# Kernel optimization log

Measured on AMD Instinct MI355X. Metric: run time of the kernel, lower is better.

## Reference

```python
import jax, jax.numpy as jnp
import numpy as np

N_NODES = 50000
IN_CH = 256
OUT_CH = 128
HID = 2 * OUT_CH  # 256
N_EDGES = 800000


def setup_inputs() -> dict:
    key = jax.random.key(0)
    ks = jax.random.split(key, 12)
    glorot = lambda k, shape: jax.random.normal(k, shape, jnp.float32) * (2.0 / sum(shape)) ** 0.5
    return {
        "x": jax.random.normal(ks[0], (N_NODES, IN_CH), jnp.float32),
        "edge_index": jax.random.randint(ks[1], (2, N_EDGES), 0, N_NODES),
        "conv_w": glorot(ks[2], (IN_CH, HID)),      # MetaGCNConv weight: x @ W
        "conv_b": jnp.zeros((HID,), jnp.float32),
        "fc1_w": glorot(ks[3], (HID, HID)), "fc1_b": jnp.zeros((HID,), jnp.float32),
        "fc2_w": glorot(ks[4], (HID, HID)), "fc2_b": jnp.zeros((HID,), jnp.float32),
        "fc3_w": glorot(ks[5], (OUT_CH, HID)), "fc3_b": jnp.zeros((OUT_CH,), jnp.float32),
        "fc4_w": glorot(ks[6], (OUT_CH, HID)), "fc4_b": jnp.zeros((OUT_CH,), jnp.float32),
    }


def reference(x, edge_index, conv_w, conv_b, fc1_w, fc1_b, fc2_w, fc2_b, fc3_w, fc3_b, fc4_w, fc4_b):
    N = x.shape[0]
    # GCN with added self-loops and symmetric normalization (PyG GCNConv semantics)
    loop = jnp.arange(N)
    src = jnp.concatenate([edge_index[0], loop])
    dst = jnp.concatenate([edge_index[1], loop])
    xw = x @ conv_w  # [N, HID]
    ones = jnp.ones_like(src, dtype=x.dtype)
    deg = jax.ops.segment_sum(ones, src, num_segments=N)
    dinv = jnp.where(deg > 0, jax.lax.rsqrt(deg), 0.0)
    norm = dinv[src] * dinv[dst]  # [E+N]
    agg = jax.ops.segment_sum(norm[:, None] * xw[src], dst, num_segments=N)  # [N, HID]
    h = jax.nn.relu(agg + conv_b)
    s = h.sum(0)  # [HID]
    lin = lambda v, w, b: jnp.tanh(v @ w.T + b)
    return (lin(s, fc1_w, fc1_b), lin(s, fc2_w, fc2_b), lin(s, fc3_w, fc3_b), lin(s, fc4_w, fc4_b))
```

## Files before the change

kernel.cpp:

```cpp
#include <hip/hip_runtime.h>
#include <math.h>

#define CH 256
#define BCAP 64

typedef short bf16x8 __attribute__((ext_vector_type(8)));
typedef float f32x4 __attribute__((ext_vector_type(4)));
typedef unsigned int u32;

__device__ __forceinline__ unsigned short f2bf(float f) {
    u32 u = __float_as_uint(f);
    u += 0x7FFFu + ((u >> 16) & 1u);
    return (unsigned short)(u >> 16);
}
__device__ __forceinline__ float bf2f(unsigned short h) {
    return __uint_as_float(((u32)h) << 16);
}
__device__ __forceinline__ float lo16f(u32 q) { return __uint_as_float(q << 16); }
__device__ __forceinline__ float hi16f(u32 q) { return __uint_as_float(q & 0xffff0000u); }
__device__ __forceinline__ u32 pkbf(float a, float b) {
    u32 ua = __float_as_uint(a) + 0x8000u;
    u32 ub = __float_as_uint(b) + 0x8000u;
    return __builtin_amdgcn_perm(ub, ua, 0x07060302u);
}
__device__ __forceinline__ void async16(const void* g, void* l) {
    __builtin_amdgcn_global_load_lds((const __attribute__((address_space(1))) u32*)g,
                                     (__attribute__((address_space(3))) u32*)l, 16, 0, 0);
}

__global__ __launch_bounds__(256) void prep_kernel(const float* __restrict__ W,
                                                   unsigned short* __restrict__ whiT,
                                                   unsigned short* __restrict__ wloT,
                                                   float4* __restrict__ zbase,
                                                   int zcount4) {
    int b = blockIdx.x, t = threadIdx.x;
    if (b < 64) {
#pragma unroll
        for (int i = 0; i < 4; i++) {
            int n = b * 4 + i;
            float w = W[(size_t)t * CH + n];
            unsigned short hi = f2bf(w);
            unsigned short lo = f2bf(w - bf2f(hi));
            whiT[(size_t)n * CH + t] = hi;
            wloT[(size_t)n * CH + t] = lo;
        }
    } else {
        int i = (b - 64) * 256 + t;
        int stride = 104 * 256;
        float4 z = make_float4(0.f, 0.f, 0.f, 0.f);
        for (; i < zcount4; i += stride) zbase[i] = z;
    }
}

__global__ __launch_bounds__(256) void mega_kernel(const float* __restrict__ x,
                                                   const unsigned short* __restrict__ whiT,
                                                   const unsigned short* __restrict__ wloT,
                                                   const int* __restrict__ ei,
                                                   unsigned* __restrict__ cnt_src,
                                                   unsigned* __restrict__ cnt_dst,
                                                   unsigned* __restrict__ col,
                                                   unsigned short* __restrict__ y,
                                                   int M, int E, int G) {
    int b = blockIdx.x, t = threadIdx.x;
    if (b < 2 * G && !(b & 1)) {
        __shared__ __align__(16) unsigned short smA [128 * 32];
        __shared__ __align__(16) unsigned short smBh[128 * 32];
        __shared__ __align__(16) unsigned short smBl[128 * 32];
        int g = b >> 1;
        int lane = t & 63, w = t >> 6;
        int m0 = (g >> 1) * 128;
        int n0 = (g & 1) * 128;
        int mo = (w >> 1) * 64, no = (w & 1) * 64;
        int quad = lane >> 4, l16 = lane & 15;

        f32x4 acc[4][4] = {};

        int arow = t >> 1, ahalf = t & 1;
        int gm = min(m0 + arow, M - 1);
        const float* xrow = x + (size_t)gm * CH + ahalf * 16;
        int idx0 = t, idx1 = t + 256;
        size_t gb0 = (size_t)(n0 + (idx0 >> 2)) * CH + (idx0 & 3) * 8;
        size_t gb1 = (size_t)(n0 + (idx1 >> 2)) * CH + (idx1 & 3) * 8;

        for (int k0 = 0; k0 < CH; k0 += 32) {
            const float4* xp = (const float4*)(xrow + k0);
            float4 v0 = xp[0], v1 = xp[1], v2 = xp[2], v3 = xp[3];
            async16(&whiT[gb0 + k0], &smBh[idx0 * 8]);
            async16(&whiT[gb1 + k0], &smBh[idx1 * 8]);
            async16(&wloT[gb0 + k0], &smBl[idx0 * 8]);
            async16(&wloT[gb1 + k0], &smBl[idx1 * 8]);
            uint4 w0 = make_uint4(pkbf(v0.x, v0.y), pkbf(v0.z, v0.w),
                                  pkbf(v1.x, v1.y), pkbf(v1.z, v1.w));
            uint4 w1 = make_uint4(pkbf(v2.x, v2.y), pkbf(v2.z, v2.w),
                                  pkbf(v3.x, v3.y), pkbf(v3.z, v3.w));
            *(uint4*)&smA[arow * 32 + ahalf * 16]     = w0;
            *(uint4*)&smA[arow * 32 + ahalf * 16 + 8] = w1;
            __syncthreads();

            bf16x8 a[4], bh[4], bl[4];
#pragma unroll
            for (int i = 0; i < 4; i++)
                a[i] = *(const bf16x8*)&smA[(mo + i * 16 + l16) * 32 + quad * 8];
#pragma unroll
            for (int j = 0; j < 4; j++) {
                bh[j] = *(const bf16x8*)&smBh[(no + j * 16 + l16) * 32 + quad * 8];
                bl[j] = *(const bf16x8*)&smBl[(no + j * 16 + l16) * 32 + quad * 8];
            }
#pragma unroll
            for (int i = 0; i < 4; i++)
#pragma unroll
                for (int j = 0; j < 4; j++) {
                    acc[i][j] = __builtin_amdgcn_mfma_f32_16x16x32_bf16(a[i], bh[j], acc[i][j], 0, 0, 0);
                    acc[i][j] = __builtin_amdgcn_mfma_f32_16x16x32_bf16(a[i], bl[j], acc[i][j], 0, 0, 0);
                }
            __syncthreads();
        }
#pragma unroll
        for (int i = 0; i < 4; i++) {
            int mbase = m0 + mo + i * 16 + quad * 4;
#pragma unroll
            for (int r = 0; r < 4; r++) {
                int m = mbase + r;
                if (m < M) {
#pragma unroll
                    for (int j = 0; j < 4; j++) {
                        int ncol = n0 + no + j * 16 + l16;
                        int s = ncol >> 5, c = ncol & 31;
                        y[((size_t)s * M + m) * 32 + c] = f2bf(acc[i][j][r]);
                    }
                }
            }
        }
    } else {
        int fb = (b < 2 * G) ? (b >> 1) : (b - G);
        if (fb >= 1024) return;
        int i = fb * 256 + t;
        int stride = 1024 * 256;
        for (; i < E; i += stride) {
            int s = ei[i];
            int d = ei[E + i];
            atomicAdd(&cnt_src[s], 1u);
            unsigned pos = atomicAdd(&cnt_dst[d], 1u);
            if (pos < BCAP) col[(size_t)d * BCAP + pos] = (unsigned)s;
        }
    }
}

__global__ __launch_bounds__(256) void dinv_kernel(const unsigned* __restrict__ cnt_src,
                                                   float* __restrict__ dinv, int N) {
    int base = (blockIdx.x * 256 + threadIdx.x) * 4;
#pragma unroll
    for (int j = 0; j < 4; j++) {
        int i = base + j;
        if (i < N) dinv[i] = rsqrtf((float)(cnt_src[i] + 1u));
    }
}

__global__ __launch_bounds__(256) void gather_kernel(const unsigned short* __restrict__ y,
                                                     const float* __restrict__ dinv,
                                                     const unsigned* __restrict__ cnt_dst,
                                                     const unsigned* __restrict__ col,
                                                     const float* __restrict__ bias,
                                                     float* __restrict__ s_sum, int N) {
    int t = threadIdx.x;
    int lane = t & 63, wv = t >> 6;
    int slice = blockIdx.x & 7;
    int grp   = blockIdx.x >> 3;
    int ng = lane >> 4;
    int g  = (lane >> 2) & 3;
    int li = lane & 3;
    const unsigned short* ys = y + (size_t)slice * N * 32;

    float b8[8];
#pragma unroll
    for (int j = 0; j < 8; j++) b8[j] = bias[slice * 32 + li * 8 + j];

    float ts[8] = {0.f, 0.f, 0.f, 0.f, 0.f, 0.f, 0.f, 0.f};

    int wid = grp * 4 + wv;
    int nw  = (gridDim.x >> 3) * 4;

    for (int base = wid * 4; base < N; base += nw * 4) {
        int n = min(base + ng, N - 1);
        unsigned deg = min(cnt_dst[n], (unsigned)BCAP);
        unsigned cnt = deg + 1;
        float gnm = (g == 0 && base + ng < N) ? 1.f : 0.f;
        unsigned mc = cnt;
        mc = max(mc, (unsigned)__shfl_xor((int)mc, 16, 64));
        mc = max(mc, (unsigned)__shfl_xor((int)mc, 32, 64));

        const unsigned* cb = col + (size_t)n * BCAP;
        float acc[8] = {0.f, 0.f, 0.f, 0.f, 0.f, 0.f, 0.f, 0.f};
        for (unsigned k = 0; k < mc; k += 4) {
            unsigned r = k + g;
            unsigned src = (r < deg) ? cb[r] : (unsigned)n;
            float wgt = (r < cnt) ? dinv[src] : 0.f;
            uint4 q = *(const uint4*)(ys + (size_t)src * 32 + li * 8);
            acc[0] = fmaf(wgt, lo16f(q.x), acc[0]);
            acc[1] = fmaf(wgt, hi16f(q.x), acc[1]);
            acc[2] = fmaf(wgt, lo16f(q.y), acc[2]);
            acc[3] = fmaf(wgt, hi16f(q.y), acc[3]);
            acc[4] = fmaf(wgt, lo16f(q.z), acc[4]);
            acc[5] = fmaf(wgt, hi16f(q.z), acc[5]);
            acc[6] = fmaf(wgt, lo16f(q.w), acc[6]);
            acc[7] = fmaf(wgt, hi16f(q.w), acc[7]);
        }
        float dvn = dinv[n];
#pragma unroll
        for (int j = 0; j < 8; j++) {
            float v = acc[j];
            v += __shfl_xor(v, 4, 64);
            v += __shfl_xor(v, 8, 64);
            float h = fmaxf(fmaf(dvn, v, b8[j]), 0.f);
            ts[j] = fmaf(gnm, h, ts[j]);
        }
    }

#pragma unroll
    for (int j = 0; j < 8; j++) {
        float v = ts[j];
        v += __shfl_xor(v, 16, 64);
        v += __shfl_xor(v, 32, 64);
        ts[j] = v;
    }

    __shared__ float red[4][32];
    if (lane < 4) {
#pragma unroll
        for (int j = 0; j < 8; j++) red[wv][lane * 8 + j] = ts[j];
    }
    __syncthreads();
    if (t < 32) {
        atomicAdd(&s_sum[slice * 32 + t],
                  red[0][t] + red[1][t] + red[2][t] + red[3][t]);
    }
}

__global__ __launch_bounds__(256) void fc_kernel(const float* __restrict__ s_sum,
                                                 const float* __restrict__ fc1_w, const float* __restrict__ fc1_b,
                                                 const float* __restrict__ fc2_w, const float* __restrict__ fc2_b,
                                                 const float* __restrict__ fc3_w, const float* __restrict__ fc3_b,
                                                 const float* __restrict__ fc4_w, const float* __restrict__ fc4_b,
                                                 float* __restrict__ out) {
    int wid  = (blockIdx.x * blockDim.x + threadIdx.x) >> 6;
    int lane = threadIdx.x & 63;
    if (wid >= 768) return;
    const float* w; const float* b; int row, obase;
    if (wid < 256)      { w = fc1_w; b = fc1_b; row = wid;       obase = 0;   }
    else if (wid < 512) { w = fc2_w; b = fc2_b; row = wid - 256; obase = 256; }
    else if (wid < 640) { w = fc3_w; b = fc3_b; row = wid - 512; obase = 512; }
    else                { w = fc4_w; b = fc4_b; row = wid - 640; obase = 640; }
    float4 wv = *(const float4*)&w[(size_t)row * 256 + lane * 4];
    float4 sv = *(const float4*)&s_sum[lane * 4];
    float d = wv.x * sv.x + wv.y * sv.y + wv.z * sv.z + wv.w * sv.w;
#pragma unroll
    for (int off = 32; off; off >>= 1) d += __shfl_down(d, off, 64);
    if (lane == 0) out[obase + row] = tanhf(d + b[row]);
}

extern "C" void kernel_launch(void* const* d_in, const int* in_sizes, int n_in,
                              void* d_out, int out_size, void* d_ws, size_t ws_size,
                              hipStream_t stream) {
    const float* x      = (const float*)d_in[0];
    const int*   ei     = (const int*)d_in[1];
    const float* conv_w = (const float*)d_in[2];
    const float* conv_b = (const float*)d_in[3];
    const float* fc1_w  = (const float*)d_in[4];
    const float* fc1_b  = (const float*)d_in[5];
    const float* fc2_w  = (const float*)d_in[6];
    const float* fc2_b  = (const float*)d_in[7];
    const float* fc3_w  = (const float*)d_in[8];
    const float* fc3_b  = (const float*)d_in[9];
    const float* fc4_w  = (const float*)d_in[10];
    const float* fc4_b  = (const float*)d_in[11];
    float* out = (float*)d_out;

    const int N = in_sizes[0] / CH;
    const int E = in_sizes[1] / 2;
    const int G = ((N + 127) / 128) * 2;

    char* ws = (char*)d_ws;
    size_t off = 0;
    auto alloc = [&](size_t bytes) -> void* {
        off = (off + 255) & ~(size_t)255;
        void* p = ws + off;
        off += bytes;
        return p;
    };
    unsigned* cnt_src = (unsigned*)alloc((size_t)N * 4);
    unsigned* cnt_dst = (unsigned*)alloc((size_t)N * 4);
    float*    s_sum   = (float*)alloc((size_t)CH * 4);
    size_t zero_bytes = off;
    unsigned* col     = (unsigned*)alloc((size_t)N * BCAP * 4);
    float*    dinv    = (float*)alloc((size_t)N * 4);
    unsigned short* whiT = (unsigned short*)alloc((size_t)CH * CH * 2);
    unsigned short* wloT = (unsigned short*)alloc((size_t)CH * CH * 2);
    unsigned short* y    = (unsigned short*)alloc((size_t)N * CH * 2);

    int zcount4 = (int)((zero_bytes + 15) / 16);

    prep_kernel<<<168, 256, 0, stream>>>(conv_w, whiT, wloT, (float4*)ws, zcount4);
    mega_kernel<<<G + 1024, 256, 0, stream>>>(x, whiT, wloT, ei,
                                              cnt_src, cnt_dst, col, y, N, E, G);
    dinv_kernel<<<(N + 1023) / 1024, 256, 0, stream>>>(cnt_src, dinv, N);
    gather_kernel<<<2048, 256, 0, stream>>>(y, dinv, cnt_dst, col, conv_b, s_sum, N);
    fc_kernel<<<192, 256, 0, stream>>>(s_sum,
                                       fc1_w, fc1_b, fc2_w, fc2_b,
                                       fc3_w, fc3_b, fc4_w, fc4_b, out);
}
```

Baseline: 260.6 us.

## Fuse dinv into gather and run FC layers in last-arriving gather blocks

Removes the separate dinv kernel by computing rsqrt(deg+1) from cnt_src inline during the gather. Also removes the separate FC kernel: each gather block increments a done counter, and the last 8 blocks to arrive spin until all blocks finish, then compute the 768 FC outputs. This saves two kernel launches and the dinv round trip through memory. In exchange the gather does extra rsqrt work and cnt_src lookups, and the tail blocks spin-wait, which is safe only because the waiting blocks are the last to arrive.

```diff
diff --git a/kernel.cpp b/kernel.cpp
--- a/kernel.cpp
+++ b/kernel.cpp
@@ -3,6 +3,7 @@
 
 #define CH 256
 #define BCAP 64
+#define GGRID 2048
 
 typedef short bf16x8 __attribute__((ext_vector_type(8)));
 typedef float f32x4 __attribute__((ext_vector_type(4)));
@@ -28,11 +29,11 @@
                                      (__attribute__((address_space(3))) u32*)l, 16, 0, 0);
 }
 
-__global__ __launch_bounds__(256) void prep_kernel(const float* __restrict__ W,
-                                                   unsigned short* __restrict__ whiT,
-                                                   unsigned short* __restrict__ wloT,
-                                                   float4* __restrict__ zbase,
-                                                   int zcount4) {
+__global__ __launch_bounds__(256) void prep0_kernel(const float* __restrict__ W,
+                                                    unsigned short* __restrict__ whiT,
+                                                    unsigned short* __restrict__ wloT,
+                                                    float4* __restrict__ zbase,
+                                                    int zcount4) {
     int b = blockIdx.x, t = threadIdx.x;
     if (b < 64) {
 #pragma unroll
@@ -46,7 +47,7 @@
         }
     } else {
         int i = (b - 64) * 256 + t;
-        int stride = 104 * 256;
+        int stride = 64 * 256;
         float4 z = make_float4(0.f, 0.f, 0.f, 0.f);
         for (; i < zcount4; i += stride) zbase[i] = z;
     }
@@ -146,26 +147,24 @@
     }
 }
 
-__global__ __launch_bounds__(256) void dinv_kernel(const unsigned* __restrict__ cnt_src,
-                                                   float* __restrict__ dinv, int N) {
-    int base = (blockIdx.x * 256 + threadIdx.x) * 4;
-#pragma unroll
-    for (int j = 0; j < 4; j++) {
-        int i = base + j;
-        if (i < N) dinv[i] = rsqrtf((float)(cnt_src[i] + 1u));
-    }
-}
-
-__global__ __launch_bounds__(256) void gather_kernel(const unsigned short* __restrict__ y,
-                                                     const float* __restrict__ dinv,
-                                                     const unsigned* __restrict__ cnt_dst,
-                                                     const unsigned* __restrict__ col,
-                                                     const float* __restrict__ bias,
-                                                     float* __restrict__ s_sum, int N) {
+__global__ __launch_bounds__(256) void gatherfc_kernel(
+        const unsigned short* __restrict__ y,
+        const unsigned* __restrict__ cnt_src,
+        const unsigned* __restrict__ cnt_dst,
+        const unsigned* __restrict__ col,
+        const float* __restrict__ bias,
+        float* __restrict__ s_sum,
+        unsigned* __restrict__ done,
+        const float* __restrict__ fc1_w, const float* __restrict__ fc1_b,
+        const float* __restrict__ fc2_w, const float* __restrict__ fc2_b,
+        const float* __restrict__ fc3_w, const float* __restrict__ fc3_b,
+        const float* __restrict__ fc4_w, const float* __restrict__ fc4_b,
+        float* __restrict__ out, int N) {
     int t = threadIdx.x;
     int lane = t & 63, wv = t >> 6;
-    int slice = blockIdx.x & 7;
-    int grp   = blockIdx.x >> 3;
+    int b = blockIdx.x;
+    int slice = b & 7;
+    int grp   = b >> 3;
     int ng = lane >> 4;
     int g  = (lane >> 2) & 3;
     int li = lane & 3;
@@ -178,7 +177,7 @@
     float ts[8] = {0.f, 0.f, 0.f, 0.f, 0.f, 0.f, 0.f, 0.f};
 
     int wid = grp * 4 + wv;
-    int nw  = (gridDim.x >> 3) * 4;
+    int nw  = (GGRID >> 3) * 4;
 
     for (int base = wid * 4; base < N; base += nw * 4) {
         int n = min(base + ng, N - 1);
@@ -194,7 +193,7 @@
         for (unsigned k = 0; k < mc; k += 4) {
             unsigned r = k + g;
             unsigned src = (r < deg) ? cb[r] : (unsigned)n;
-            float wgt = (r < cnt) ? dinv[src] : 0.f;
+            float wgt = (r < cnt) ? rsqrtf((float)(cnt_src[src] + 1u)) : 0.f;
             uint4 q = *(const uint4*)(ys + (size_t)src * 32 + li * 8);
             acc[0] = fmaf(wgt, lo16f(q.x), acc[0]);
             acc[1] = fmaf(wgt, hi16f(q.x), acc[1]);
@@ -205,7 +204,7 @@
             acc[6] = fmaf(wgt, lo16f(q.w), acc[6]);
             acc[7] = fmaf(wgt, hi16f(q.w), acc[7]);
         }
-        float dvn = dinv[n];
+        float dvn = rsqrtf((float)(cnt_src[n] + 1u));
 #pragma unroll
         for (int j = 0; j < 8; j++) {
             float v = acc[j];
@@ -234,28 +233,38 @@
         atomicAdd(&s_sum[slice * 32 + t],
                   red[0][t] + red[1][t] + red[2][t] + red[3][t]);
     }
-}
-
-__global__ __launch_bounds__(256) void fc_kernel(const float* __restrict__ s_sum,
-                                                 const float* __restrict__ fc1_w, const float* __restrict__ fc1_b,
-                                                 const float* __restrict__ fc2_w, const float* __restrict__ fc2_b,
-                                                 const float* __restrict__ fc3_w, const float* __restrict__ fc3_b,
-                                                 const float* __restrict__ fc4_w, const float* __restrict__ fc4_b,
-                                                 float* __restrict__ out) {
-    int wid  = (blockIdx.x * blockDim.x + threadIdx.x) >> 6;
-    int lane = threadIdx.x & 63;
-    if (wid >= 768) return;
-    const float* w; const float* b; int row, obase;
-    if (wid < 256)      { w = fc1_w; b = fc1_b; row = wid;       obase = 0;   }
-    else if (wid < 512) { w = fc2_w; b = fc2_b; row = wid - 256; obase = 256; }
-    else if (wid < 640) { w = fc3_w; b = fc3_b; row = wid - 512; obase = 512; }
-    else                { w = fc4_w; b = fc4_b; row = wid - 640; obase = 640; }
-    float4 wv = *(const float4*)&w[(size_t)row * 256 + lane * 4];
-    float4 sv = *(const float4*)&s_sum[lane * 4];
-    float d = wv.x * sv.x + wv.y * sv.y + wv.z * sv.z + wv.w * sv.w;
-#pragma unroll
-    for (int off = 32; off; off >>= 1) d += __shfl_down(d, off, 64);
-    if (lane == 0) out[obase + row] = tanhf(d + b[row]);
+
+    __threadfence();
+    __syncthreads();
+    __shared__ unsigned sold;
+    if (t == 0)
+        sold = __hip_atomic_fetch_add(done, 1u, __ATOMIC_RELEASE, __HIP_MEMORY_SCOPE_AGENT);
+    __syncthreads();
+    unsigned old = sold;
+    if (old >= GGRID - 8) {
+        if (t == 0) {
+            while (__hip_atomic_load(done, __ATOMIC_ACQUIRE, __HIP_MEMORY_SCOPE_AGENT) < GGRID)
+                __builtin_amdgcn_s_sleep(16);
+        }
+        __syncthreads();
+        __threadfence();
+        int share = (int)(old - (GGRID - 8));
+#pragma unroll
+        for (int o = 0; o < 24; o++) {
+            int wid2 = share * 96 + wv * 24 + o;
+            const float* w; const float* bb; int row, obase;
+            if (wid2 < 256)      { w = fc1_w; bb = fc1_b; row = wid2;       obase = 0;   }
+            else if (wid2 < 512) { w = fc2_w; bb = fc2_b; row = wid2 - 256; obase = 256; }
+            else if (wid2 < 640) { w = fc3_w; bb = fc3_b; row = wid2 - 512; obase = 512; }
+            else                 { w = fc4_w; bb = fc4_b; row = wid2 - 640; obase = 640; }
+            float4 wv4 = *(const float4*)&w[(size_t)row * 256 + lane * 4];
+            float4 sv  = *(const float4*)&s_sum[lane * 4];
+            float d = wv4.x * sv.x + wv4.y * sv.y + wv4.z * sv.z + wv4.w * sv.w;
+#pragma unroll
+            for (int off = 32; off; off >>= 1) d += __shfl_down(d, off, 64);
+            if (lane == 0) out[obase + row] = tanhf(d + bb[row]);
+        }
+    }
 }
 
 extern "C" void kernel_launch(void* const* d_in, const int* in_sizes, int n_in,
@@ -290,21 +299,21 @@
     unsigned* cnt_src = (unsigned*)alloc((size_t)N * 4);
     unsigned* cnt_dst = (unsigned*)alloc((size_t)N * 4);
     float*    s_sum   = (float*)alloc((size_t)CH * 4);
-    size_t zero_bytes = off;
+    unsigned* done    = (unsigned*)alloc(256);
+    size_t zbytes = off;
     unsigned* col     = (unsigned*)alloc((size_t)N * BCAP * 4);
-    float*    dinv    = (float*)alloc((size_t)N * 4);
     unsigned short* whiT = (unsigned short*)alloc((size_t)CH * CH * 2);
     unsigned short* wloT = (unsigned short*)alloc((size_t)CH * CH * 2);
     unsigned short* y    = (unsigned short*)alloc((size_t)N * CH * 2);
 
-    int zcount4 = (int)((zero_bytes + 15) / 16);
-
-    prep_kernel<<<168, 256, 0, stream>>>(conv_w, whiT, wloT, (float4*)ws, zcount4);
+    int zcount4 = (int)((zbytes + 15) / 16);
+
+    prep0_kernel<<<128, 256, 0, stream>>>(conv_w, whiT, wloT, (float4*)ws, zcount4);
     mega_kernel<<<G + 1024, 256, 0, stream>>>(x, whiT, wloT, ei,
                                               cnt_src, cnt_dst, col, y, N, E, G);
-    dinv_kernel<<<(N + 1023) / 1024, 256, 0, stream>>>(cnt_src, dinv, N);
-    gather_kernel<<<2048, 256, 0, stream>>>(y, dinv, cnt_dst, col, conv_b, s_sum, N);
-    fc_kernel<<<192, 256, 0, stream>>>(s_sum,
-                                       fc1_w, fc1_b, fc2_w, fc2_b,
-                                       fc3_w, fc3_b, fc4_w, fc4_b, out);
-}
+    gatherfc_kernel<<<GGRID, 256, 0, stream>>>(y, cnt_src, cnt_dst, col, conv_b,
+                                               s_sum, done,
+                                               fc1_w, fc1_b, fc2_w, fc2_b,
+                                               fc3_w, fc3_b, fc4_w, fc4_b,
+                                               out, N);
+}
```

Measured after the change: 442.9 us. +69.9%, slower.
